# Performance work log

Measured on AMD Instinct MI355X. Metric: run time of the kernel, lower is better.

Reference implementation:

```python
import jax, jax.numpy as jnp
import numpy as np

B, T, IN, H = 32, 256, 64, 128
TOP_K = 5
TRUNC = 100   # truncate_length: detach h,c every TRUNC steps
EPS = 1e-7
NEG = -1e9


def setup_inputs() -> dict:
    key = jax.random.key(0)
    ks = jax.random.split(key, 6)
    s = 1.0 / np.sqrt(H)  # torch LSTMCell default init bound
    xav = float(1.414 * np.sqrt(6.0 / (2 * H + 1)))  # xavier_uniform gain=1.414
    return {
        "x": jax.random.normal(ks[0], (B, T, IN), jnp.float32),
        "W_ih": jax.random.uniform(ks[1], (4 * H, IN), jnp.float32, -s, s),
        "W_hh": jax.random.uniform(ks[2], (4 * H, H), jnp.float32, -s, s),
        "b_ih": jax.random.uniform(ks[3], (4 * H,), jnp.float32, -s, s),
        "b_hh": jax.random.uniform(ks[4], (4 * H,), jnp.float32, -s, s),
        "w_t": jax.random.uniform(ks[5], (2 * H, 1), jnp.float32, -xav, xav),
    }


def _lstm_cell(x_t, h, c, W_ih, W_hh, b_ih, b_hh):
    # torch gate order: i, f, g, o
    g = x_t @ W_ih.T + h @ W_hh.T + (b_ih + b_hh)
    i, f, gg, o = jnp.split(g, 4, axis=-1)
    c = jax.nn.sigmoid(f) * c + jax.nn.sigmoid(i) * jnp.tanh(gg)
    h = jax.nn.sigmoid(o) * jnp.tanh(c)
    return h, c


def reference(x, W_ih, W_hh, b_ih, b_hh, w_t):
    Bv, Tv, _ = x.shape
    Hh = W_hh.shape[1]
    # score = w_t . tanh(cat(h_t, h_old)) splits additively since tanh is elementwise
    w_a = w_t[:Hh, 0]
    w_b = w_t[Hh:, 0]
    pos = jnp.arange(Tv + 1)

    def step(carry, inp):
        h, c, h_old = carry          # h_old: [B, T+1, H], slot 0 = initial zeros
        i, x_t = inp
        det = ((i + 1) % TRUNC) == 0
        h = jnp.where(det, jax.lax.stop_gradient(h), h)
        c = jnp.where(det, jax.lax.stop_gradient(c), c)
        h, c = _lstm_cell(x_t, h, c, W_ih, W_hh, b_ih, b_hh)
        rem = i + 1                  # remember_size
        mask = pos < rem             # [T+1] valid memory slots
        # attention scores over stored states
        s = (jnp.tanh(h) @ w_a)[:, None] + jnp.tanh(h_old) @ w_b  # [B, T+1]
        s_valid = jnp.where(mask[None, :], s, NEG)
        delta = jax.lax.top_k(s_valid, TOP_K)[0][:, -1] + EPS
        w_sp = jnp.clip(s_valid - delta[:, None], 0.0)
        w_sp = w_sp / (w_sp.sum(axis=1, keepdims=True) + EPS)
        # Sparse_attention returns raw scores when remember_size <= top_k
        attn_w = jnp.where(rem <= TOP_K, s, w_sp)
        attn_c = jnp.einsum('bt,bth->bh', jnp.where(mask[None, :], attn_w, 0.0), h_old)
        h = h + attn_c
        h_old = jax.lax.dynamic_update_slice(h_old, h[:, None, :], (0, rem, 0))
        return (h, c, h_old), (attn_c, attn_w)

    h0 = jnp.zeros((Bv, Hh), x.dtype)
    c0 = jnp.zeros((Bv, Hh), x.dtype)
    buf0 = jnp.zeros((Bv, Tv + 1, Hh), x.dtype)
    xs = (jnp.arange(Tv), jnp.swapaxes(x, 0, 1))
    _, (attn_c_all, attn_w_all) = jax.lax.scan(step, (h0, c0, buf0), xs)
    # module returns last step's (attn_c, out_attn_w); final remember_size == T
    return attn_c_all[-1], attn_w_all[-1][:, :Tv, None]
```

## Files before the change

kernel.cpp:

```cpp
#include <hip/hip_runtime.h>
#include <math.h>

#define NEGF -1000000000.0f
#define EPSF 1e-7f


typedef float v4f __attribute__((ext_vector_type(4)));
#define FMA4(a, b, c) __builtin_elementwise_fma((a), (b), (c))

#define RAWBAR() asm volatile("s_waitcnt lgkmcnt(0)\n\ts_barrier" ::: "memory")

__device__ __forceinline__ float fsigmoid(float x) {
  return 1.0f / (1.0f + __expf(-x));
}
__device__ __forceinline__ float ftanh(float x) {
  return 1.0f - 2.0f / (1.0f + __expf(2.0f * x));
}

__device__ __forceinline__ float wave_allsum(float v) {
#if __has_builtin(__builtin_amdgcn_update_dpp) && __has_builtin(__builtin_amdgcn_readlane)
  float f = v;
#define DPPSTEP(ctrl, rmask) { \
    int t = __builtin_amdgcn_update_dpp(0, __builtin_bit_cast(int, f), \
                                        ctrl, rmask, 0xf, true); \
    f += __builtin_bit_cast(float, t); }
  DPPSTEP(0x111, 0xf)
  DPPSTEP(0x112, 0xf)
  DPPSTEP(0x114, 0xf)
  DPPSTEP(0x118, 0xf)
  DPPSTEP(0x142, 0xa)
  DPPSTEP(0x143, 0x8)
#undef DPPSTEP
  return __builtin_bit_cast(float,
      __builtin_amdgcn_readlane(__builtin_bit_cast(int, f), 63));
#else
  for (int off = 1; off < 64; off <<= 1) v += __shfl_xor(v, off, 64);
  return v;
#endif
}

__global__ __launch_bounds__(512) void xw_kernel(
    const float* __restrict__ x, const float* __restrict__ W_ih,
    const float* __restrict__ b_ih, const float* __restrict__ b_hh,
    float* __restrict__ xw)
{
  const int t0 = blockIdx.x * 32;
  const int b  = blockIdx.y;
  const int g  = threadIdx.x;

  __shared__ float sx[32 * 64];
  ((float4*)sx)[threadIdx.x] =
      ((const float4*)(x + (size_t)(b * 256 + t0) * 64))[threadIdx.x];

  const float4* wr = (const float4*)(W_ih + (size_t)g * 64);
  float4 w0 = wr[0],  w1 = wr[1],  w2 = wr[2],  w3 = wr[3],
         w4 = wr[4],  w5 = wr[5],  w6 = wr[6],  w7 = wr[7],
         w8 = wr[8],  w9 = wr[9],  w10 = wr[10], w11 = wr[11],
         w12 = wr[12], w13 = wr[13], w14 = wr[14], w15 = wr[15];
  const float bias = b_ih[g] + b_hh[g];
  __syncthreads();

  float* dst = xw + (size_t)(b * 256 + t0) * 512 + g;
  for (int tt = 0; tt < 32; ++tt) {
    const float4* xr = (const float4*)(sx + tt * 64);
    float a0 = 0.0f, a1 = 0.0f, a2 = 0.0f, a3 = 0.0f;
#define XSTEP(j) { float4 hv = xr[j]; \
    a0 = fmaf(w##j.x, hv.x, a0); a1 = fmaf(w##j.y, hv.y, a1); \
    a2 = fmaf(w##j.z, hv.z, a2); a3 = fmaf(w##j.w, hv.w, a3); }
    XSTEP(0) XSTEP(1) XSTEP(2) XSTEP(3) XSTEP(4) XSTEP(5) XSTEP(6) XSTEP(7)
    XSTEP(8) XSTEP(9) XSTEP(10) XSTEP(11) XSTEP(12) XSTEP(13) XSTEP(14) XSTEP(15)
#undef XSTEP
    dst[(size_t)tt * 512] = (a0 + a1) + (a2 + a3) + bias;
  }
}

__global__
__attribute__((amdgpu_flat_work_group_size(512, 512), amdgpu_waves_per_eu(2, 2)))
void lstm_attn(
    const float* __restrict__ xw, const float* __restrict__ W_hh,
    const float* __restrict__ w_t, float* __restrict__ out)
{
  const int b   = blockIdx.x;
  const int tid = threadIdx.x;
  const int l   = tid & 63;
  const int wid = tid >> 6;
  const int p   = tid & 127;
  const int q   = tid >> 7;

  __shared__ float ho[257 * 128];
  __shared__ float sh_part[4 * 512];
  __shared__ float sh_d[8];
  __shared__ float sh_pa[2];
  __shared__ float sh_dn[2];

  const v4f* pI = (const v4f*)(W_hh + (size_t)(p      ) * 128 + (q << 5));
  const v4f* pF = (const v4f*)(W_hh + (size_t)(p + 128) * 128 + (q << 5));
  const v4f* pG = (const v4f*)(W_hh + (size_t)(p + 256) * 128 + (q << 5));
  const v4f* pO = (const v4f*)(W_hh + (size_t)(p + 384) * 128 + (q << 5));
  v4f wI0 = pI[0], wI1 = pI[1], wI2 = pI[2], wI3 = pI[3],
      wI4 = pI[4], wI5 = pI[5], wI6 = pI[6], wI7 = pI[7];
  v4f wF0 = pF[0], wF1 = pF[1], wF2 = pF[2], wF3 = pF[3],
      wF4 = pF[4], wF5 = pF[5], wF6 = pF[6], wF7 = pF[7];
  v4f wG0 = pG[0], wG1 = pG[1], wG2 = pG[2], wG3 = pG[3],
      wG4 = pG[4], wG5 = pG[5], wG6 = pG[6], wG7 = pG[7];
  v4f wO0 = pO[0], wO1 = pO[1], wO2 = pO[2], wO3 = pO[3],
      wO4 = pO[4], wO5 = pO[5], wO6 = pO[6], wO7 = pO[7];

  const int j = (wid << 6) + l;
  float cc = 0.0f;
  float wa = 0.0f, wb = 0.0f;
  float t5v0 = 0.0f, t5v1 = NEGF, t5v2 = NEGF, t5v3 = NEGF, t5v4 = NEGF;
  int   t5i0 = 0, t5i1 = 0, t5i2 = 0, t5i3 = 0;
  float gn0 = 0.0f, gn1 = 0.0f, gn2 = 0.0f, gn3 = 0.0f;
  int   ofs0 = 0, ofs1 = 0, ofs2 = 0, ofs3 = 0;

  if (wid < 2) {
    wa = w_t[j]; wb = w_t[128 + j];
    ho[j] = 0.0f;
    __builtin_amdgcn_s_setprio(1);
  }
  if (tid == 0) sh_d[0] = 0.0f;
  __syncthreads();

  const float* xwb = xw + (size_t)b * 256 * 512;
  float xcI = 0.0f, xcF = 0.0f, xcG = 0.0f, xcO = 0.0f;
  if (q == 0) {
    xcI = xwb[p];       xcF = xwb[p + 128];
    xcG = xwb[p + 256]; xcO = xwb[p + 384];
  }

  for (int i = 0; i < 256; ++i) {
    const int rem = i + 1;

    v4f aI = {xcI, 0.0f, 0.0f, 0.0f};
    v4f aF = {xcF, 0.0f, 0.0f, 0.0f};
    v4f aG = {xcG, 0.0f, 0.0f, 0.0f};
    v4f aO = {xcO, 0.0f, 0.0f, 0.0f};
    if (q == 0 && i < 255) {
      const float* xn = xwb + (size_t)(i + 1) * 512;
      xcI = xn[p];       xcF = xn[p + 128];
      xcG = xn[p + 256]; xcO = xn[p + 384];
    }
    const v4f* hh4 = (const v4f*)(ho + i * 128 + (q << 5));
#define KS(k) { v4f hv = hh4[k]; \
    aI = FMA4(wI##k, hv, aI); aF = FMA4(wF##k, hv, aF); \
    aG = FMA4(wG##k, hv, aG); aO = FMA4(wO##k, hv, aO); }
    KS(0) KS(1) KS(2) KS(3) KS(4) KS(5) KS(6) KS(7)
#undef KS
    {
      float* sp = sh_part + (q << 9) + p;
      sp[0]   = (aI.x + aI.y) + (aI.z + aI.w);
      sp[128] = (aF.x + aF.y) + (aF.z + aF.w);
      sp[256] = (aG.x + aG.y) + (aG.z + aG.w);
      sp[384] = (aO.x + aO.y) + (aO.z + aO.w);
    }

    float hv0 = 0.0f, hv1 = 0.0f, hv2 = 0.0f, hv3 = 0.0f;
    if (wid < 2 && i >= 5) {
      hv0 = ho[ofs0]; hv1 = ho[ofs1]; hv2 = ho[ofs2]; hv3 = ho[ofs3];
    }
    RAWBAR();

    float hc = 0.0f, at = 0.0f;
    if (wid < 2) {
      const float* s0 = sh_part + j;
      float Pi = (s0[0]         + s0[512])         + (s0[1024]         + s0[1536]);
      float Pf = (s0[128]       + s0[640])         + (s0[1152]         + s0[1664]);
      float Pg = (s0[256]       + s0[768])         + (s0[1280]         + s0[1792]);
      float Po = (s0[384]       + s0[896])         + (s0[1408]         + s0[1920]);
      cc = fsigmoid(Pf) * cc + fsigmoid(Pi) * ftanh(Pg);
      hc = fsigmoid(Po) * ftanh(cc);
    }
    if (i < 5) {
      if (wid < 2) {
        float pa = wave_allsum(ftanh(hc) * wa);
        if (l == 0) sh_pa[wid] = pa;
      }
      RAWBAR();
      if (wid < 2) {
        float a = sh_pa[0] + sh_pa[1];
        at = 0.0f;
        for (int t = 0; t <= i; ++t)
          at = fmaf(a + sh_d[t], ho[t * 128 + j], at);
      }
    } else if (wid < 2) {
      at = gn0 * hv0;
      at = fmaf(gn1, hv1, at);
      at = fmaf(gn2, hv2, at);
      at = fmaf(gn3, hv3, at);
    }
    if (wid < 2) {
      float hn = hc + at;
      ho[rem * 128 + j] = hn;
      float pdn = wave_allsum(ftanh(hn) * wb);
      if (l == 0) sh_dn[wid] = pdn;
      if (i == 255) {
        out[b * 128 + j] = at;
        if (wid == 0) {
          #pragma unroll
          for (int m = 0; m < 4; ++m) {
            int t = l + 64 * m;
            float val = 0.0f;
            if (t == t5i0) val = gn0;
            if (t == t5i1) val = gn1;
            if (t == t5i2) val = gn2;
            if (t == t5i3) val = gn3;
            out[4096 + b * 256 + t] = val;
          }
        }
      }
    }
    RAWBAR();

    if (wid < 2 && i < 255) {
      float dn = sh_dn[0] + sh_dn[1];
      if (wid == 0 && l == 0 && i < 4) sh_d[rem] = dn;
      float v = dn; int vi = rem;
      if (v > t5v0) { float tv = t5v0; int ti = t5i0; t5v0 = v; t5i0 = vi; v = tv; vi = ti; }
      if (v > t5v1) { float tv = t5v1; int ti = t5i1; t5v1 = v; t5i1 = vi; v = tv; vi = ti; }
      if (v > t5v2) { float tv = t5v2; int ti = t5i2; t5v2 = v; t5i2 = vi; v = tv; vi = ti; }
      if (v > t5v3) { float tv = t5v3; int ti = t5i3; t5v3 = v; t5i3 = vi; v = tv; vi = ti; }
      if (v > t5v4) { t5v4 = v; }
      float g0 = fmaxf(t5v0 - t5v4 - EPSF, 0.0f);
      float g1 = fmaxf(t5v1 - t5v4 - EPSF, 0.0f);
      float g2 = fmaxf(t5v2 - t5v4 - EPSF, 0.0f);
      float g3 = fmaxf(t5v3 - t5v4 - EPSF, 0.0f);
      float inv = 1.0f / (((g0 + g1) + (g2 + g3)) + EPSF);
      gn0 = g0 * inv; gn1 = g1 * inv; gn2 = g2 * inv; gn3 = g3 * inv;
      ofs0 = (t5i0 << 7) + j; ofs1 = (t5i1 << 7) + j;
      ofs2 = (t5i2 << 7) + j; ofs3 = (t5i3 << 7) + j;
    }
  }
}

extern "C" void kernel_launch(void* const* d_in, const int* in_sizes, int n_in,
                              void* d_out, int out_size, void* d_ws, size_t ws_size,
                              hipStream_t stream) {
  const float* x    = (const float*)d_in[0];
  const float* W_ih = (const float*)d_in[1];
  const float* W_hh = (const float*)d_in[2];
  const float* b_ih = (const float*)d_in[3];
  const float* b_hh = (const float*)d_in[4];
  const float* w_t  = (const float*)d_in[5];
  float* out = (float*)d_out;

  float* xw = (float*)d_ws;

  xw_kernel<<<dim3(8, 32), 512, 0, stream>>>(x, W_ih, b_ih, b_hh, xw);
  lstm_attn<<<dim3(32), 512, 0, stream>>>(xw, W_hh, w_t, out);
}
```

Baseline: 367.5 us.

## Split recurrent matvec into 2 K-chunks with 2 gate rows per thread

Changes the W_hh work split so each thread owns two gate rows over a 64-wide slice of the hidden vector, instead of four gate rows over a 32-wide slice. Each step's cross-thread partial sum then has 2 partials per gate instead of 4. This halves the shared-memory partial buffer and the reduction reads on the critical path between the matvec and the cell update. In exchange each thread does a longer dependent FMA chain per accumulator, with fewer independent accumulators to hide latency.

```diff
diff --git a/kernel.cpp b/kernel.cpp
--- a/kernel.cpp
+++ b/kernel.cpp
@@ -84,27 +84,25 @@
   const int tid = threadIdx.x;
   const int l   = tid & 63;
   const int wid = tid >> 6;
-  const int p   = tid & 127;
-  const int q   = tid >> 7;
+  const int g2  = tid & 255;
+  const int q   = tid >> 8;
 
   __shared__ float ho[257 * 128];
-  __shared__ float sh_part[4 * 512];
+  __shared__ float sh_part[2 * 512];
   __shared__ float sh_d[8];
   __shared__ float sh_pa[2];
   __shared__ float sh_dn[2];
 
-  const v4f* pI = (const v4f*)(W_hh + (size_t)(p      ) * 128 + (q << 5));
-  const v4f* pF = (const v4f*)(W_hh + (size_t)(p + 128) * 128 + (q << 5));
-  const v4f* pG = (const v4f*)(W_hh + (size_t)(p + 256) * 128 + (q << 5));
-  const v4f* pO = (const v4f*)(W_hh + (size_t)(p + 384) * 128 + (q << 5));
-  v4f wI0 = pI[0], wI1 = pI[1], wI2 = pI[2], wI3 = pI[3],
-      wI4 = pI[4], wI5 = pI[5], wI6 = pI[6], wI7 = pI[7];
-  v4f wF0 = pF[0], wF1 = pF[1], wF2 = pF[2], wF3 = pF[3],
-      wF4 = pF[4], wF5 = pF[5], wF6 = pF[6], wF7 = pF[7];
-  v4f wG0 = pG[0], wG1 = pG[1], wG2 = pG[2], wG3 = pG[3],
-      wG4 = pG[4], wG5 = pG[5], wG6 = pG[6], wG7 = pG[7];
-  v4f wO0 = pO[0], wO1 = pO[1], wO2 = pO[2], wO3 = pO[3],
-      wO4 = pO[4], wO5 = pO[5], wO6 = pO[6], wO7 = pO[7];
+  const v4f* pA = (const v4f*)(W_hh + (size_t)g2 * 128 + (q << 6));
+  const v4f* pB = (const v4f*)(W_hh + (size_t)(g2 + 256) * 128 + (q << 6));
+  v4f wA0 = pA[0],  wA1 = pA[1],  wA2 = pA[2],  wA3 = pA[3],
+      wA4 = pA[4],  wA5 = pA[5],  wA6 = pA[6],  wA7 = pA[7],
+      wA8 = pA[8],  wA9 = pA[9],  wA10 = pA[10], wA11 = pA[11],
+      wA12 = pA[12], wA13 = pA[13], wA14 = pA[14], wA15 = pA[15];
+  v4f wB0 = pB[0],  wB1 = pB[1],  wB2 = pB[2],  wB3 = pB[3],
+      wB4 = pB[4],  wB5 = pB[5],  wB6 = pB[6],  wB7 = pB[7],
+      wB8 = pB[8],  wB9 = pB[9],  wB10 = pB[10], wB11 = pB[11],
+      wB12 = pB[12], wB13 = pB[13], wB14 = pB[14], wB15 = pB[15];
 
   const int j = (wid << 6) + l;
   float cc = 0.0f;
@@ -123,36 +121,28 @@
   __syncthreads();
 
   const float* xwb = xw + (size_t)b * 256 * 512;
-  float xcI = 0.0f, xcF = 0.0f, xcG = 0.0f, xcO = 0.0f;
-  if (q == 0) {
-    xcI = xwb[p];       xcF = xwb[p + 128];
-    xcG = xwb[p + 256]; xcO = xwb[p + 384];
-  }
+  float xcA = 0.0f, xcB = 0.0f;
+  if (q == 0) { xcA = xwb[g2]; xcB = xwb[g2 + 256]; }
 
   for (int i = 0; i < 256; ++i) {
     const int rem = i + 1;
 
-    v4f aI = {xcI, 0.0f, 0.0f, 0.0f};
-    v4f aF = {xcF, 0.0f, 0.0f, 0.0f};
-    v4f aG = {xcG, 0.0f, 0.0f, 0.0f};
-    v4f aO = {xcO, 0.0f, 0.0f, 0.0f};
+    v4f aA = {xcA, 0.0f, 0.0f, 0.0f};
+    v4f aB = {xcB, 0.0f, 0.0f, 0.0f};
     if (q == 0 && i < 255) {
       const float* xn = xwb + (size_t)(i + 1) * 512;
-      xcI = xn[p];       xcF = xn[p + 128];
-      xcG = xn[p + 256]; xcO = xn[p + 384];
-    }
-    const v4f* hh4 = (const v4f*)(ho + i * 128 + (q << 5));
+      xcA = xn[g2]; xcB = xn[g2 + 256];
+    }
+    const v4f* hh4 = (const v4f*)(ho + i * 128 + (q << 6));
 #define KS(k) { v4f hv = hh4[k]; \
-    aI = FMA4(wI##k, hv, aI); aF = FMA4(wF##k, hv, aF); \
-    aG = FMA4(wG##k, hv, aG); aO = FMA4(wO##k, hv, aO); }
+    aA = FMA4(wA##k, hv, aA); aB = FMA4(wB##k, hv, aB); }
     KS(0) KS(1) KS(2) KS(3) KS(4) KS(5) KS(6) KS(7)
+    KS(8) KS(9) KS(10) KS(11) KS(12) KS(13) KS(14) KS(15)
 #undef KS
     {
-      float* sp = sh_part + (q << 9) + p;
-      sp[0]   = (aI.x + aI.y) + (aI.z + aI.w);
-      sp[128] = (aF.x + aF.y) + (aF.z + aF.w);
-      sp[256] = (aG.x + aG.y) + (aG.z + aG.w);
-      sp[384] = (aO.x + aO.y) + (aO.z + aO.w);
+      float* sp = sh_part + (q << 9) + g2;
+      sp[0]   = (aA.x + aA.y) + (aA.z + aA.w);
+      sp[256] = (aB.x + aB.y) + (aB.z + aB.w);
     }
 
     float hv0 = 0.0f, hv1 = 0.0f, hv2 = 0.0f, hv3 = 0.0f;
@@ -164,10 +154,10 @@
     float hc = 0.0f, at = 0.0f;
     if (wid < 2) {
       const float* s0 = sh_part + j;
-      float Pi = (s0[0]         + s0[512])         + (s0[1024]         + s0[1536]);
-      float Pf = (s0[128]       + s0[640])         + (s0[1152]         + s0[1664]);
-      float Pg = (s0[256]       + s0[768])         + (s0[1280]         + s0[1792]);
-      float Po = (s0[384]       + s0[896])         + (s0[1408]         + s0[1920]);
+      float Pi = s0[0]   + s0[512];
+      float Pf = s0[128] + s0[640];
+      float Pg = s0[256] + s0[768];
+      float Po = s0[384] + s0[896];
       cc = fsigmoid(Pf) * cc + fsigmoid(Pi) * ftanh(Pg);
       hc = fsigmoid(Po) * ftanh(cc);
     }
@@ -223,10 +213,10 @@
       if (v > t5v4) { t5v4 = v; }
       float g0 = fmaxf(t5v0 - t5v4 - EPSF, 0.0f);
       float g1 = fmaxf(t5v1 - t5v4 - EPSF, 0.0f);
-      float g2 = fmaxf(t5v2 - t5v4 - EPSF, 0.0f);
+      float g2f = fmaxf(t5v2 - t5v4 - EPSF, 0.0f);
       float g3 = fmaxf(t5v3 - t5v4 - EPSF, 0.0f);
-      float inv = 1.0f / (((g0 + g1) + (g2 + g3)) + EPSF);
-      gn0 = g0 * inv; gn1 = g1 * inv; gn2 = g2 * inv; gn3 = g3 * inv;
+      float inv = 1.0f / (((g0 + g1) + (g2f + g3)) + EPSF);
+      gn0 = g0 * inv; gn1 = g1 * inv; gn2 = g2f * inv; gn3 = g3 * inv;
       ofs0 = (t5i0 << 7) + j; ofs1 = (t5i1 << 7) + j;
       ofs2 = (t5i2 << 7) + j; ofs3 = (t5i3 << 7) + j;
     }
```

Result: no change. 368.1 us (median of 2 runs) (+0.2%).
